# Performance work log

Hardware: AMD Instinct MI355X
Metric: run time of the kernel (lower is better)

Reference implementation:

```python
import jax, jax.numpy as jnp
import numpy as np

S_RANGE = 15
BLOCK = 4


def _avg_pool(x, k, stride):
    # x: [B,H,W,C], VALID padding (keras AveragePooling2D default)
    s = jax.lax.reduce_window(x, 0.0, jax.lax.add,
                              (1, k, k, 1), (1, stride, stride, 1), 'VALID')
    return s / float(k * k)


def setup_inputs() -> dict:
    key = jax.random.key(0)
    k1, k2 = jax.random.split(key)
    B, H, W, C = 4, 128, 128, 128
    features_0 = jax.random.normal(k1, (B, H, W, C), dtype=jnp.float32)
    features_0from1 = jax.random.normal(k2, (B, H, W, C), dtype=jnp.float32)
    return {"features_0": features_0, "features_0from1": features_0from1}


def reference(features_0, features_0from1):
    B, H, W, C = features_0.shape
    Hc, Wc = H // BLOCK, W // BLOCK

    # f_c: AvgPool(4, stride 4) -> [B,Hc,Wc,C]
    f_c = _avg_pool(features_0, BLOCK, BLOCK)
    # f_r: AvgPool(4, stride 1, VALID) -> [B,H-3,W-3,C]
    f_r = _avg_pool(features_0from1, BLOCK, 1)

    # tf.image.extract_patches(15x15, stride 4, SAME) zero-pads (S_RANGE-1)/2=7 each side
    pad = (S_RANGE - 1) // 2
    f_r_pad = jnp.pad(f_r, ((0, 0), (pad, S_RANGE - 1 - pad),
                            (pad, S_RANGE - 1 - pad), (0, 0)))

    # Gather all 15x15 windows at stride 4: patches[b,i,u,j,v,c] = f_r_pad[b,4i+u,4j+v,c]
    idx_h = BLOCK * jnp.arange(Hc)[:, None] + jnp.arange(S_RANGE)[None, :]  # [Hc,15]
    idx_w = BLOCK * jnp.arange(Wc)[:, None] + jnp.arange(S_RANGE)[None, :]  # [Wc,15]
    patches = f_r_pad[:, idx_h]           # [B,Hc,15,Wpad,C]
    patches = patches[:, :, :, idx_w]     # [B,Hc,15,Wc,15,C]

    # cost: mean over channels of f_c[b,i,j,:] * window values -> [B,15,15,Hc,Wc]
    corr = jnp.einsum('bijc,biujvc->buvij', f_c, patches) / C
    corr = jax.nn.leaky_relu(corr, 0.1)

    # nearest-neighbor upsample by BLOCK; displacement d = u*S_RANGE + v goes last
    cv = jnp.repeat(jnp.repeat(corr, BLOCK, axis=3), BLOCK, axis=4)  # [B,15,15,H,W]
    cv = cv.reshape(B, S_RANGE * S_RANGE, H, W).transpose(0, 2, 3, 1)  # [B,H,W,225]
    return cv
```

## Files before the change

kernel.cpp:

```cpp
#include <hip/hip_runtime.h>
#include <hip/hip_bf16.h>

#define B_   4
#define Hf   128
#define Wf   128
#define HC   32
#define WC   32
#define SR   15
#define PAD  7
#define FR   125
#define FRP  139

typedef float vfloat4 __attribute__((ext_vector_type(4)));
typedef _Float16 half2v __attribute__((ext_vector_type(2)));

static __device__ __forceinline__ unsigned short f2h(float x) {
    _Float16 h = (_Float16)x;
    unsigned short u; __builtin_memcpy(&u, &h, 2); return u;
}

static __device__ __forceinline__ float mrg(float x, float y, bool hi, int m) {
    float u0 = hi ? x : y;
    float t  = __shfl_xor(u0, m, 64);
    return (hi ? y : x) + t;
}

__global__ __launch_bounds__(256) void pool_fc(const float* __restrict__ in0,
                                               float* __restrict__ fc) {
    int t = blockIdx.x * 256 + threadIdx.x;
    int c4 = t & 31;
    int j  = (t >> 5) & 31;
    int i  = (t >> 10) & 31;
    int b  = t >> 15;
    const float4* in = reinterpret_cast<const float4*>(in0);
    size_t base = ((size_t)(b * Hf + 4 * i) * Wf + 4 * j) * 32 + c4;
    float4 acc = make_float4(0.f, 0.f, 0.f, 0.f);
#pragma unroll
    for (int dy = 0; dy < 4; ++dy)
#pragma unroll
        for (int dx = 0; dx < 4; ++dx) {
            float4 v = in[base + dy * (Wf * 32) + dx * 32];
            acc.x += v.x; acc.y += v.y; acc.z += v.z; acc.w += v.w;
        }
    const float s = 1.0f / 16.0f;
    acc.x *= s; acc.y *= s; acc.z *= s; acc.w *= s;
    reinterpret_cast<float4*>(fc)[t] = acc;
}

__global__ __launch_bounds__(256) void pool_fr(const float* __restrict__ in1,
                                               unsigned short* __restrict__ fr16) {
    int bid = blockIdx.x;
    int yt = bid % 18;
    int xt = (bid / 18) % 18;
    int b  = bid / (18 * 18);
    int c4 = threadIdx.x & 31;
    int x  = xt * 8 + (threadIdx.x >> 5);
    if (x >= FRP) return;
    int y0 = yt * 8;
    bool xin = (x >= PAD) && (x < PAD + FR);

    float4 h[11];
    if (xin) {
        int xi = x - PAD;
        const float4* base = reinterpret_cast<const float4*>(in1) + (size_t)(b * Hf * Wf) * 32 + c4;
#pragma unroll
        for (int k = 0; k < 11; ++k) {
            int r = y0 - PAD + k;
            r = r < 0 ? 0 : (r > Hf - 1 ? Hf - 1 : r);
            float4 s = make_float4(0.f, 0.f, 0.f, 0.f);
#pragma unroll
            for (int dx = 0; dx < 4; ++dx) {
                float4 v = base[(size_t)(r * Wf + xi + dx) * 32];
                s.x += v.x; s.y += v.y; s.z += v.z; s.w += v.w;
            }
            h[k] = s;
        }
    }
    const float s = 1.0f / 16.0f;
    ushort4* fr4 = reinterpret_cast<ushort4*>(fr16);
#pragma unroll
    for (int yy = 0; yy < 8; ++yy) {
        int y = y0 + yy;
        if (y >= FRP) continue;
        ushort4 o = make_ushort4(0, 0, 0, 0);
        if (xin && y >= PAD && y < PAD + FR) {
            o.x = f2h((h[yy].x + h[yy+1].x + h[yy+2].x + h[yy+3].x) * s);
            o.y = f2h((h[yy].y + h[yy+1].y + h[yy+2].y + h[yy+3].y) * s);
            o.z = f2h((h[yy].z + h[yy+1].z + h[yy+2].z + h[yy+3].z) * s);
            o.w = f2h((h[yy].w + h[yy+1].w + h[yy+2].w + h[yy+3].w) * s);
        }
        fr4[((size_t)(b * FRP + y) * FRP + x) * 32 + c4] = o;
    }
}

__global__ __launch_bounds__(256) void corr_kernel(const float* __restrict__ fc,
                                                   const unsigned short* __restrict__ fr16,
                                                   float* __restrict__ out) {
    int blk  = blockIdx.x;
    int cell = (blk & 7) * 512 + (blk >> 3);
    int j = cell & 31;
    int i = (cell >> 5) & 31;
    int b = cell >> 10;

    int tid = threadIdx.x;
    int g   = tid >> 5;
    int gl  = tid & 31;

    __shared__ float corr_rep[900];

    float4 f = reinterpret_cast<const float4*>(fc)[((b * HC + i) * WC + j) * 32 + gl];
    half2v f01 = { (_Float16)f.x, (_Float16)f.y };
    half2v f23 = { (_Float16)f.z, (_Float16)f.w };

    const uint2* frbase = reinterpret_cast<const uint2*>(fr16);
    bool h16 = gl & 16, h8 = gl & 8, h4 = gl & 4, h2 = gl & 2;
    int vidx = ((gl >> 4) & 1) * 8 + ((gl >> 3) & 1) * 4 + ((gl >> 2) & 1) * 2 + ((gl >> 1) & 1);

#pragma unroll
    for (int pass = 0; pass < 2; ++pass) {
        int u = g + pass * 8;
        if (u < SR) {
            int row = 4 * i + u;
            const uint2* p = frbase + ((size_t)(b * FRP + row) * FRP + 4 * j) * 32 + gl;

            float a[16];
            a[15] = 0.f;
#pragma unroll
            for (int v = 0; v < SR; ++v) {
                uint2 w = p[v * 32];
                half2v w01 = __builtin_bit_cast(half2v, w.x);
                half2v w23 = __builtin_bit_cast(half2v, w.y);
                float d = __builtin_amdgcn_fdot2(w01, f01, 0.0f, false);
                a[v] = __builtin_amdgcn_fdot2(w23, f23, d, false);
            }

            float bb[8], cc[4], dd[2], e;
#pragma unroll
            for (int k = 0; k < 8; ++k) bb[k] = mrg(a[k], a[k + 8], h16, 16);
#pragma unroll
            for (int k = 0; k < 4; ++k) cc[k] = mrg(bb[k], bb[k + 4], h8, 8);
#pragma unroll
            for (int k = 0; k < 2; ++k) dd[k] = mrg(cc[k], cc[k + 2], h4, 4);
            e = mrg(dd[0], dd[1], h2, 2);
            e += __shfl_xor(e, 1, 64);

            if (vidx < SR) {
                float cv = e * (1.0f / 128.0f);
                float val = cv > 0.f ? cv : 0.1f * cv;
                int uvq = u * SR + vidx;
                int c0 = (gl & 1) * 225;
                corr_rep[c0 + uvq] = val;
                corr_rep[c0 + 450 + uvq] = val;
            }
        }
    }
    __syncthreads();

    if (tid < SR * SR) {
        vfloat4 val = *reinterpret_cast<const vfloat4*>(&corr_rep[4 * tid]);
        vfloat4* out4 = reinterpret_cast<vfloat4*>(out);
        long pix   = (long)(b * Hf + 4 * i) * Wf + 4 * j;
        long base4 = pix * (SR * SR) / 4;
#pragma unroll
        for (int di = 0; di < 4; ++di)
            __builtin_nontemporal_store(val, &out4[base4 + di * (Wf * SR * SR / 4) + tid]);
    }
}

extern "C" void kernel_launch(void* const* d_in, const int* in_sizes, int n_in,
                              void* d_out, int out_size, void* d_ws, size_t ws_size,
                              hipStream_t stream) {
    const float* f0 = (const float*)d_in[0];
    const float* f1 = (const float*)d_in[1];
    float* out = (float*)d_out;

    float* fc = (float*)d_ws;
    unsigned short* fr16 = (unsigned short*)(fc + B_ * HC * WC * 128);

    pool_fc<<<512, 256, 0, stream>>>(f0, fc);
    pool_fr<<<4 * 18 * 18, 256, 0, stream>>>(f1, fr16);
    corr_kernel<<<B_ * HC * WC, 256, 0, stream>>>(fc, fr16, out);
}
```

Baseline: 46.74 us.

## Move 4x4 average pooling of f_r after the channel dot product

Instead of pooling features_0from1 with a 4x4 box filter before the correlation, the first kernel now only converts the padded raw input to fp16 and merges the f_c pooling into the same launch. The correlation kernel computes dot products against an 18x18 window of raw pixels, then applies the separable 4x4 box sum in shared memory and masks positions outside the valid pooled region. This uses linearity to avoid the pooling pass and its intermediate buffer, and drops one kernel launch. In exchange the correlation kernel does more loads and dot products per cell (18x18 instead of 15x15) and adds extra shared-memory passes and barriers.

```diff
diff --git a/kernel.cpp b/kernel.cpp
--- a/kernel.cpp
+++ b/kernel.cpp
@@ -1,5 +1,4 @@
 #include <hip/hip_runtime.h>
-#include <hip/hip_bf16.h>
 
 #define B_   4
 #define Hf   128
@@ -9,7 +8,8 @@
 #define SR   15
 #define PAD  7
 #define FR   125
-#define FRP  139
+#define PH   142
+#define PW   144
 
 typedef float vfloat4 __attribute__((ext_vector_type(4)));
 typedef _Float16 half2v __attribute__((ext_vector_type(2)));
@@ -25,77 +25,56 @@
     return (hi ? y : x) + t;
 }
 
-__global__ __launch_bounds__(256) void pool_fc(const float* __restrict__ in0,
-                                               float* __restrict__ fc) {
-    int t = blockIdx.x * 256 + threadIdx.x;
-    int c4 = t & 31;
-    int j  = (t >> 5) & 31;
-    int i  = (t >> 10) & 31;
-    int b  = t >> 15;
-    const float4* in = reinterpret_cast<const float4*>(in0);
-    size_t base = ((size_t)(b * Hf + 4 * i) * Wf + 4 * j) * 32 + c4;
-    float4 acc = make_float4(0.f, 0.f, 0.f, 0.f);
+__global__ __launch_bounds__(256) void poolcvt(const float* __restrict__ in0,
+                                               const float* __restrict__ in1,
+                                               float* __restrict__ fc,
+                                               unsigned short* __restrict__ in1h) {
+    int bid = blockIdx.x;
+    if (bid < 4 * 18 * 18) {
+        int yt = bid % 18;
+        int xt = (bid / 18) % 18;
+        int b  = bid / 324;
+        int c4 = threadIdx.x & 31;
+        int x  = xt * 8 + (threadIdx.x >> 5);
+        bool xin = (x >= PAD) && (x < PAD + Wf);
+        const float4* src = reinterpret_cast<const float4*>(in1) + (size_t)(b * Hf * Wf) * 32 + c4;
+        ushort4* dst = reinterpret_cast<ushort4*>(in1h);
 #pragma unroll
-    for (int dy = 0; dy < 4; ++dy)
+        for (int yy = 0; yy < 8; ++yy) {
+            int y = yt * 8 + yy;
+            if (y >= PH) continue;
+            ushort4 o = make_ushort4(0, 0, 0, 0);
+            if (xin && y >= PAD && y < PAD + Hf) {
+                float4 v = src[(size_t)((y - PAD) * Wf + (x - PAD)) * 32];
+                o.x = f2h(v.x); o.y = f2h(v.y); o.z = f2h(v.z); o.w = f2h(v.w);
+            }
+            dst[((size_t)(b * PH + y) * PW + x) * 32 + c4] = o;
+        }
+    } else {
+        int t = (bid - 4 * 18 * 18) * 256 + threadIdx.x;
+        int c4 = t & 31;
+        int j  = (t >> 5) & 31;
+        int i  = (t >> 10) & 31;
+        int b  = t >> 15;
+        const float4* in = reinterpret_cast<const float4*>(in0);
+        size_t base = ((size_t)(b * Hf + 4 * i) * Wf + 4 * j) * 32 + c4;
+        float4 acc = make_float4(0.f, 0.f, 0.f, 0.f);
 #pragma unroll
-        for (int dx = 0; dx < 4; ++dx) {
-            float4 v = in[base + dy * (Wf * 32) + dx * 32];
-            acc.x += v.x; acc.y += v.y; acc.z += v.z; acc.w += v.w;
-        }
-    const float s = 1.0f / 16.0f;
-    acc.x *= s; acc.y *= s; acc.z *= s; acc.w *= s;
-    reinterpret_cast<float4*>(fc)[t] = acc;
-}
-
-__global__ __launch_bounds__(256) void pool_fr(const float* __restrict__ in1,
-                                               unsigned short* __restrict__ fr16) {
-    int bid = blockIdx.x;
-    int yt = bid % 18;
-    int xt = (bid / 18) % 18;
-    int b  = bid / (18 * 18);
-    int c4 = threadIdx.x & 31;
-    int x  = xt * 8 + (threadIdx.x >> 5);
-    if (x >= FRP) return;
-    int y0 = yt * 8;
-    bool xin = (x >= PAD) && (x < PAD + FR);
-
-    float4 h[11];
-    if (xin) {
-        int xi = x - PAD;
-        const float4* base = reinterpret_cast<const float4*>(in1) + (size_t)(b * Hf * Wf) * 32 + c4;
-#pragma unroll
-        for (int k = 0; k < 11; ++k) {
-            int r = y0 - PAD + k;
-            r = r < 0 ? 0 : (r > Hf - 1 ? Hf - 1 : r);
-            float4 s = make_float4(0.f, 0.f, 0.f, 0.f);
+        for (int dy = 0; dy < 4; ++dy)
 #pragma unroll
             for (int dx = 0; dx < 4; ++dx) {
-                float4 v = base[(size_t)(r * Wf + xi + dx) * 32];
-                s.x += v.x; s.y += v.y; s.z += v.z; s.w += v.w;
+                float4 v = in[base + dy * (Wf * 32) + dx * 32];
+                acc.x += v.x; acc.y += v.y; acc.z += v.z; acc.w += v.w;
             }
-            h[k] = s;
-        }
-    }
-    const float s = 1.0f / 16.0f;
-    ushort4* fr4 = reinterpret_cast<ushort4*>(fr16);
-#pragma unroll
-    for (int yy = 0; yy < 8; ++yy) {
-        int y = y0 + yy;
-        if (y >= FRP) continue;
-        ushort4 o = make_ushort4(0, 0, 0, 0);
-        if (xin && y >= PAD && y < PAD + FR) {
-            o.x = f2h((h[yy].x + h[yy+1].x + h[yy+2].x + h[yy+3].x) * s);
-            o.y = f2h((h[yy].y + h[yy+1].y + h[yy+2].y + h[yy+3].y) * s);
-            o.z = f2h((h[yy].z + h[yy+1].z + h[yy+2].z + h[yy+3].z) * s);
-            o.w = f2h((h[yy].w + h[yy+1].w + h[yy+2].w + h[yy+3].w) * s);
-        }
-        fr4[((size_t)(b * FRP + y) * FRP + x) * 32 + c4] = o;
+        const float sc = 1.0f / 16.0f;
+        acc.x *= sc; acc.y *= sc; acc.z *= sc; acc.w *= sc;
+        reinterpret_cast<float4*>(fc)[t] = acc;
     }
 }
 
-__global__ __launch_bounds__(256) void corr_kernel(const float* __restrict__ fc,
-                                                   const unsigned short* __restrict__ fr16,
-                                                   float* __restrict__ out) {
+__global__ __launch_bounds__(256) void corr_g(const float* __restrict__ fc,
+                                              const unsigned short* __restrict__ in1h,
+                                              float* __restrict__ out) {
     int blk  = blockIdx.x;
     int cell = (blk & 7) * 512 + (blk >> 3);
     int j = cell & 31;
@@ -106,58 +85,75 @@
     int g   = tid >> 5;
     int gl  = tid & 31;
 
-    __shared__ float corr_rep[900];
+    __shared__ float g_s[18][20];
+    __shared__ float h_s[18][16];
+    __shared__ float rep[900];
 
     float4 f = reinterpret_cast<const float4*>(fc)[((b * HC + i) * WC + j) * 32 + gl];
     half2v f01 = { (_Float16)f.x, (_Float16)f.y };
     half2v f23 = { (_Float16)f.z, (_Float16)f.w };
 
-    const uint2* frbase = reinterpret_cast<const uint2*>(fr16);
+    const uint2* base = reinterpret_cast<const uint2*>(in1h)
+                        + ((size_t)(b * PH + 4 * i) * PW + 4 * j) * 32 + gl;
+
     bool h16 = gl & 16, h8 = gl & 8, h4 = gl & 4, h2 = gl & 2;
     int vidx = ((gl >> 4) & 1) * 8 + ((gl >> 3) & 1) * 4 + ((gl >> 2) & 1) * 2 + ((gl >> 1) & 1);
 
+    int nrows = (g < 2) ? 3 : 2;
+    for (int rr = 0; rr < nrows; ++rr) {
+        int row = g + rr * 8;
+        const uint2* p = base + (size_t)row * (PW * 32);
+
+        float a[18];
 #pragma unroll
-    for (int pass = 0; pass < 2; ++pass) {
-        int u = g + pass * 8;
-        if (u < SR) {
-            int row = 4 * i + u;
-            const uint2* p = frbase + ((size_t)(b * FRP + row) * FRP + 4 * j) * 32 + gl;
+        for (int s = 0; s < 18; ++s) {
+            uint2 w = p[s * 32];
+            half2v w01 = __builtin_bit_cast(half2v, w.x);
+            half2v w23 = __builtin_bit_cast(half2v, w.y);
+            float d = __builtin_amdgcn_fdot2(w01, f01, 0.0f, false);
+            a[s] = __builtin_amdgcn_fdot2(w23, f23, d, false);
+        }
 
-            float a[16];
-            a[15] = 0.f;
+        float bb[8], cc[4], dd[2], e;
 #pragma unroll
-            for (int v = 0; v < SR; ++v) {
-                uint2 w = p[v * 32];
-                half2v w01 = __builtin_bit_cast(half2v, w.x);
-                half2v w23 = __builtin_bit_cast(half2v, w.y);
-                float d = __builtin_amdgcn_fdot2(w01, f01, 0.0f, false);
-                a[v] = __builtin_amdgcn_fdot2(w23, f23, d, false);
-            }
+        for (int k = 0; k < 8; ++k) bb[k] = mrg(a[k], a[k + 8], h16, 16);
+#pragma unroll
+        for (int k = 0; k < 4; ++k) cc[k] = mrg(bb[k], bb[k + 4], h8, 8);
+#pragma unroll
+        for (int k = 0; k < 2; ++k) dd[k] = mrg(cc[k], cc[k + 2], h4, 4);
+        e = mrg(dd[0], dd[1], h2, 2);
+        e += __shfl_xor(e, 1, 64);
+        if (!(gl & 1)) g_s[row][vidx] = e;
 
-            float bb[8], cc[4], dd[2], e;
+        float e16 = a[16], e17 = a[17];
 #pragma unroll
-            for (int k = 0; k < 8; ++k) bb[k] = mrg(a[k], a[k + 8], h16, 16);
-#pragma unroll
-            for (int k = 0; k < 4; ++k) cc[k] = mrg(bb[k], bb[k + 4], h8, 8);
-#pragma unroll
-            for (int k = 0; k < 2; ++k) dd[k] = mrg(cc[k], cc[k + 2], h4, 4);
-            e = mrg(dd[0], dd[1], h2, 2);
-            e += __shfl_xor(e, 1, 64);
-
-            if (vidx < SR) {
-                float cv = e * (1.0f / 128.0f);
-                float val = cv > 0.f ? cv : 0.1f * cv;
-                int uvq = u * SR + vidx;
-                int c0 = (gl & 1) * 225;
-                corr_rep[c0 + uvq] = val;
-                corr_rep[c0 + 450 + uvq] = val;
-            }
+        for (int m = 1; m <= 16; m <<= 1) {
+            e16 += __shfl_xor(e16, m, 64);
+            e17 += __shfl_xor(e17, m, 64);
         }
+        if (gl == 0) { g_s[row][16] = e16; g_s[row][17] = e17; }
     }
     __syncthreads();
 
-    if (tid < SR * SR) {
-        vfloat4 val = *reinterpret_cast<const vfloat4*>(&corr_rep[4 * tid]);
+    for (int q = tid; q < 18 * 15; q += 256) {
+        int y = q / 15, v = q % 15;
+        h_s[y][v] = g_s[y][v] + g_s[y][v + 1] + g_s[y][v + 2] + g_s[y][v + 3];
+    }
+    __syncthreads();
+
+    if (tid < 225) {
+        int u = tid / 15, v = tid % 15;
+        float s4 = h_s[u][v] + h_s[u + 1][v] + h_s[u + 2][v] + h_s[u + 3][v];
+        int r = 4 * i + u - PAD, c = 4 * j + v - PAD;
+        bool ok = (r >= 0) && (r < FR) && (c >= 0) && (c < FR);
+        float cv = s4 * (1.0f / 2048.0f);
+        float val = ok ? (cv > 0.f ? cv : 0.1f * cv) : 0.f;
+        rep[tid] = val; rep[225 + tid] = val; rep[450 + tid] = val; rep[675 + tid] = val;
+    }
+    __syncthreads();
+
+    if (tid < 225) {
+        vfloat4 val = *reinterpret_cast<const vfloat4*>(&rep[4 * tid]);
         vfloat4* out4 = reinterpret_cast<vfloat4*>(out);
         long pix   = (long)(b * Hf + 4 * i) * Wf + 4 * j;
         long base4 = pix * (SR * SR) / 4;
@@ -175,9 +171,8 @@
     float* out = (float*)d_out;
 
     float* fc = (float*)d_ws;
-    unsigned short* fr16 = (unsigned short*)(fc + B_ * HC * WC * 128);
+    unsigned short* in1h = (unsigned short*)(fc + B_ * HC * WC * 128);
 
-    pool_fc<<<512, 256, 0, stream>>>(f0, fc);
-    pool_fr<<<4 * 18 * 18, 256, 0, stream>>>(f1, fr16);
-    corr_kernel<<<B_ * HC * WC, 256, 0, stream>>>(fc, fr16, out);
+    poolcvt<<<4 * 18 * 18 + 512, 256, 0, stream>>>(f0, f1, fc, in1h);
+    corr_g<<<B_ * HC * WC, 256, 0, stream>>>(fc, in1h, out);
 }
```

After: 45.08 us. 3.6% less time.
